# Kernel tuning notes

Measured on AMD Instinct MI355X. Metric: run time of the kernel, lower is better.

The kernel has to match this reference:

```python
import jax, jax.numpy as jnp
import numpy as np

B, H, W, C = 4, 64, 64, 256
C8 = C // 8

def setup_inputs() -> dict:
    key = jax.random.key(0)
    k1, k2, k3, k4 = jax.random.split(key, 4)
    # glorot-uniform-ish init for 1x1 conv kernels stored as [Cin, Cout]
    def glorot(k, cin, cout):
        lim = np.sqrt(6.0 / (cin + cout)).astype(np.float32)
        return jax.random.uniform(k, (cin, cout), jnp.float32, -lim, lim)
    return {
        "x": jax.random.normal(k1, (B, H, W, C), jnp.float32),
        "kernel_f": glorot(k2, C, C8),
        "kernel_g": glorot(k3, C, C8),
        "kernel_h": glorot(k4, C, C),
        "gamma": jnp.zeros((1,), jnp.float32),
    }

def reference(x, kernel_f, kernel_g, kernel_h, gamma):
    b, h, w, c = x.shape
    n = h * w
    xf = x.reshape(b, n, c)                       # [B, N, C]
    # 1x1 convs == per-position matmuls
    f = jnp.einsum('bnc,cd->bnd', xf, kernel_f)   # [B, N, C/8]
    g = jnp.einsum('bnc,cd->bnd', xf, kernel_g)   # [B, N, C/8]
    hh = jnp.einsum('bnc,cd->bnd', xf, kernel_h)  # [B, N, C]
    s = jnp.einsum('bnd,bmd->bnm', g, f)          # [B, N, N]
    beta = jax.nn.softmax(s, axis=-1)
    o = jnp.einsum('bnm,bmc->bnc', beta, hh)      # [B, N, C]
    o = o.reshape(b, h, w, c)
    return gamma * o + x
```

## Files before the change

### kernel.cpp

```cpp
#include <hip/hip_runtime.h>
#include <hip/hip_bf16.h>

typedef __bf16 bf16x8 __attribute__((ext_vector_type(8)));
typedef float f32x4 __attribute__((ext_vector_type(4)));
typedef float f32x16 __attribute__((ext_vector_type(16)));
typedef unsigned short u16;
typedef unsigned int u32;

__device__ __forceinline__ u16 f2bf_rne(float f){
  union { float f; u32 u; } v; v.f = f;
  u32 r = v.u + 0x7fffu + ((v.u >> 16) & 1u);
  return (u16)(r >> 16);
}
__device__ __forceinline__ u32 pack2(float a, float b){
  return __builtin_amdgcn_perm(__float_as_uint(a), __float_as_uint(b), 0x03020706u);
}
#define BARRIER_LGKM() asm volatile("s_waitcnt lgkmcnt(0)\n\ts_barrier" ::: "memory")

__global__ __launch_bounds__(512) void prep_kernel(
    const float* __restrict__ Wf, const float* __restrict__ Wg,
    const float* __restrict__ Wh, u16* __restrict__ Wfrag){
  const int cc = blockIdx.x;
  const int t = threadIdx.x;
  const int kk = t >> 6, lane = t & 63;
  const int L = lane & 15, quad = lane >> 4;
  const int n = cc * 16 + L;
  u32 pk[4];
  #pragma unroll
  for (int j2 = 0; j2 < 4; ++j2){
    float v[2];
    #pragma unroll
    for (int h = 0; h < 2; ++h){
      int k = kk * 32 + quad * 8 + j2 * 2 + h;
      if (n < 256)      v[h] = Wh[k * 256 + n];
      else if (n < 288) v[h] = Wf[k * 32 + (n - 256)];
      else              v[h] = Wg[k * 32 + (n - 288)];
    }
    pk[j2] = (u32)f2bf_rne(v[0]) | ((u32)f2bf_rne(v[1]) << 16);
  }
  uint4* dst = (uint4*)(Wfrag + ((size_t)(cc * 8 + kk) * 64 + lane) * 8);
  *dst = make_uint4(pk[0], pk[1], pk[2], pk[3]);
}

__global__ __launch_bounds__(512) void proj_kernel(
    const float* __restrict__ x, const u16* __restrict__ Wfrag,
    u16* __restrict__ Qg, u16* __restrict__ Kg, u16* __restrict__ Vfrag)
{
  __shared__ __align__(16) u16 smem[256 * 72];
  u16 (*xb)[264] = (u16(*)[264])smem;
  u16 (*Vr)[72]  = (u16(*)[72])smem;

  const int tid = threadIdx.x;
  const int lane = tid & 63, wave = tid >> 6;
  const int L = lane & 15, quad = lane >> 4;
  const int rowgrp = wave >> 1, colhalf = wave & 1;
  const int n0 = blockIdx.x * 64;

  const float4* xsrc = (const float4*)(x + (size_t)n0 * 256);
  #pragma unroll
  for (int j = 0; j < 8; ++j){
    int idx = j * 512 + tid;
    int row = idx >> 6, col4 = idx & 63;
    float4 v = xsrc[idx];
    u32 p0 = (u32)f2bf_rne(v.x) | ((u32)f2bf_rne(v.y) << 16);
    u32 p1 = (u32)f2bf_rne(v.z) | ((u32)f2bf_rne(v.w) << 16);
    *(uint2*)&xb[row][col4 * 4] = make_uint2(p0, p1);
  }
  __syncthreads();

  f32x4 acc[10];
  #pragma unroll
  for (int cc = 0; cc < 10; ++cc) acc[cc] = (f32x4){0.f, 0.f, 0.f, 0.f};

  #pragma unroll
  for (int kk = 0; kk < 8; ++kk){
    bf16x8 a = *(const bf16x8*)&xb[rowgrp * 16 + L][kk * 32 + quad * 8];
    #pragma unroll
    for (int cc = 0; cc < 10; ++cc){
      int ccg = colhalf * 10 + cc;
      bf16x8 bfr = *(const bf16x8*)(Wfrag + ((size_t)(ccg * 8 + kk) * 64 + lane) * 8);
      acc[cc] = __builtin_amdgcn_mfma_f32_16x16x32_bf16(a, bfr, acc[cc], 0, 0, 0);
    }
  }

  if (colhalf){
    #pragma unroll
    for (int cc = 6; cc < 10; ++cc){
      int ccg = 10 + cc;
      u16* dst = (ccg < 18) ? Kg : Qg;
      float sc = (ccg < 18) ? 1.0f : 1.44269504088896f;
      int c = (ccg & 1) * 16 + L;
      #pragma unroll
      for (int r = 0; r < 4; ++r){
        int row = n0 + rowgrp * 16 + quad * 4 + r;
        dst[(size_t)row * 32 + c] = f2bf_rne(acc[cc][r] * sc);
      }
    }
  }

  __syncthreads();

  {
    const int cmax = colhalf ? 6 : 10;
    for (int cc = 0; cc < cmax; ++cc){
      int ccg = colhalf * 10 + cc;
      int c = ccg * 16 + L;
      #pragma unroll
      for (int r = 0; r < 4; ++r){
        int tn = rowgrp * 16 + quad * 4 + r;
        int p  = ((tn & 15) << 2) | (tn >> 4);
        Vr[c][p] = f2bf_rne(acc[cc][r]);
      }
    }
  }
  __syncthreads();

  u16* Vblk = Vfrag + (size_t)blockIdx.x * (256 * 64);
  #pragma unroll
  for (int i = 0; i < 4; ++i){
    int idx = i * 512 + tid;
    *(uint4*)(Vblk + (size_t)idx * 8) = *(const uint4*)&Vr[idx & 255][(idx >> 8) * 8];
  }
}

__global__ __launch_bounds__(512) void flash_kernel(
    const u16* __restrict__ Qg, const u16* __restrict__ Kg, const u16* __restrict__ Vfrag,
    const float* __restrict__ x, const float* __restrict__ gamma, float* __restrict__ out)
{
  constexpr float SH = -92.33248261689366f;
  __shared__ __align__(16) char smem[65536];
  u16 (*Plds)[2][64][72] = (u16 (*)[2][64][72])smem;
  float (*Osh)[256] = (float (*)[256])smem;
  __shared__ float Lsh[64];

  const int tid = threadIdx.x, lane = tid & 63, wave = tid >> 6;
  const int L = lane & 15, quad = lane >> 4;
  const int m32 = lane & 31, h32 = lane >> 5;
  const bool producer = wave < 4;
  const int pw = wave & 3;

  const int id = blockIdx.x;
  const int xcd = id & 7;
  const int b = xcd >> 1;
  const int qt = (xcd & 1) * 32 + (id >> 3);
  const int q0 = qt * 64;

  const u16* Qb = Qg + (size_t)(b * 4096) * 32;
  const u16* Kb = Kg + (size_t)(b * 4096) * 32;
  const u16* Vb = Vfrag + (size_t)b * (64 * 256 * 64);
  const float gm = gamma[0];

  bf16x8 qa;
  bf16x8 kcA0, kcA1, kcA2, kcA3, kcB0, kcB1, kcB2, kcB3;
  bf16x8 vfA[8], vfB[8];
  if (producer){
    qa = *(const bf16x8*)(Qb + (size_t)(q0 + pw * 16 + L) * 32 + quad * 8);
    const u16* kpA = Kb + (size_t)(0 * 64 + L) * 32 + quad * 8;
    kcA0 = *(const bf16x8*)(kpA);
    kcA1 = *(const bf16x8*)(kpA + 512);
    kcA2 = *(const bf16x8*)(kpA + 1024);
    kcA3 = *(const bf16x8*)(kpA + 1536);
    const u16* kpB = kpA + 2048;
    kcB0 = *(const bf16x8*)(kpB);
    kcB1 = *(const bf16x8*)(kpB + 512);
    kcB2 = *(const bf16x8*)(kpB + 1024);
    kcB3 = *(const bf16x8*)(kpB + 1536);
  } else {
    #pragma unroll
    for (int ks = 0; ks < 4; ++ks){
      const u16* vrow = Vb + (size_t)((ks * 2 + h32) * 256 + pw * 64 + m32) * 8;
      vfA[ks * 2]     = *(const bf16x8*)(vrow);
      vfA[ks * 2 + 1] = *(const bf16x8*)(vrow + 32 * 8);
      vfB[ks * 2]     = *(const bf16x8*)(vrow + 16384);
      vfB[ks * 2 + 1] = *(const bf16x8*)(vrow + 16384 + 32 * 8);
    }
  }

  f32x16 acc[4];
  #pragma unroll
  for (int t = 0; t < 4; ++t)
    #pragma unroll
    for (int i = 0; i < 16; ++i) acc[t][i] = 0.f;
  float lsum[4] = {0.f, 0.f, 0.f, 0.f};
  const f32x4 zero = (f32x4){0.f, 0.f, 0.f, 0.f};

  for (int it = 0; it < 32; ++it){
    u16 (*PwA)[72] = Plds[it & 1][0];
    u16 (*PwB)[72] = Plds[it & 1][1];

    if (producer){
      f32x4 sA0 = __builtin_amdgcn_mfma_f32_16x16x32_bf16(qa, kcA0, zero, 0, 0, 0);
      f32x4 sA1 = __builtin_amdgcn_mfma_f32_16x16x32_bf16(qa, kcA1, zero, 0, 0, 0);
      f32x4 sA2 = __builtin_amdgcn_mfma_f32_16x16x32_bf16(qa, kcA2, zero, 0, 0, 0);
      f32x4 sA3 = __builtin_amdgcn_mfma_f32_16x16x32_bf16(qa, kcA3, zero, 0, 0, 0);
      f32x4 sB0 = __builtin_amdgcn_mfma_f32_16x16x32_bf16(qa, kcB0, zero, 0, 0, 0);
      f32x4 sB1 = __builtin_amdgcn_mfma_f32_16x16x32_bf16(qa, kcB1, zero, 0, 0, 0);
      f32x4 sB2 = __builtin_amdgcn_mfma_f32_16x16x32_bf16(qa, kcB2, zero, 0, 0, 0);
      f32x4 sB3 = __builtin_amdgcn_mfma_f32_16x16x32_bf16(qa, kcB3, zero, 0, 0, 0);

      if (it < 31){
        const u16* kpa = Kb + (size_t)((2 * it + 2) * 64 + L) * 32 + quad * 8;
        kcA0 = *(const bf16x8*)(kpa);
        kcA1 = *(const bf16x8*)(kpa + 512);
        kcA2 = *(const bf16x8*)(kpa + 1024);
        kcA3 = *(const bf16x8*)(kpa + 1536);
        const u16* kpb = kpa + 2048;
        kcB0 = *(const bf16x8*)(kpb);
        kcB1 = *(const bf16x8*)(kpb + 512);
        kcB2 = *(const bf16x8*)(kpb + 1024);
        kcB3 = *(const bf16x8*)(kpb + 1536);
      }

      #pragma unroll
      for (int r = 0; r < 4; ++r){
        float a0 = __builtin_amdgcn_exp2f(sA0[r] + SH);
        float a1 = __builtin_amdgcn_exp2f(sA1[r] + SH);
        float a2 = __builtin_amdgcn_exp2f(sA2[r] + SH);
        float a3 = __builtin_amdgcn_exp2f(sA3[r] + SH);
        float b0 = __builtin_amdgcn_exp2f(sB0[r] + SH);
        float b1 = __builtin_amdgcn_exp2f(sB1[r] + SH);
        float b2 = __builtin_amdgcn_exp2f(sB2[r] + SH);
        float b3 = __builtin_amdgcn_exp2f(sB3[r] + SH);
        lsum[r] += ((a0 + a1) + (a2 + a3)) + ((b0 + b1) + (b2 + b3));
        *(uint2*)&PwA[pw * 16 + quad * 4 + r][L * 4] =
            make_uint2(pack2(a0, a1), pack2(a2, a3));
        *(uint2*)&PwB[pw * 16 + quad * 4 + r][L * 4] =
            make_uint2(pack2(b0, b1), pack2(b2, b3));
      }
    }

    BARRIER_LGKM();

    if (!producer){
      #pragma unroll
      for (int ks = 0; ks < 4; ++ks){
        bf16x8 af0 = *(const bf16x8*)&PwA[m32][ks * 16 + h32 * 8];
        bf16x8 af1 = *(const bf16x8*)&PwA[32 + m32][ks * 16 + h32 * 8];
        acc[0] = __builtin_amdgcn_mfma_f32_32x32x16_bf16(af0, vfA[ks*2],   acc[0], 0, 0, 0);
        acc[1] = __builtin_amdgcn_mfma_f32_32x32x16_bf16(af0, vfA[ks*2+1], acc[1], 0, 0, 0);
        acc[2] = __builtin_amdgcn_mfma_f32_32x32x16_bf16(af1, vfA[ks*2],   acc[2], 0, 0, 0);
        acc[3] = __builtin_amdgcn_mfma_f32_32x32x16_bf16(af1, vfA[ks*2+1], acc[3], 0, 0, 0);
      }
      #pragma unroll
      for (int ks = 0; ks < 4; ++ks){
        bf16x8 af0 = *(const bf16x8*)&PwB[m32][ks * 16 + h32 * 8];
        bf16x8 af1 = *(const bf16x8*)&PwB[32 + m32][ks * 16 + h32 * 8];
        acc[0] = __builtin_amdgcn_mfma_f32_32x32x16_bf16(af0, vfB[ks*2],   acc[0], 0, 0, 0);
        acc[1] = __builtin_amdgcn_mfma_f32_32x32x16_bf16(af0, vfB[ks*2+1], acc[1], 0, 0, 0);
        acc[2] = __builtin_amdgcn_mfma_f32_32x32x16_bf16(af1, vfB[ks*2],   acc[2], 0, 0, 0);
        acc[3] = __builtin_amdgcn_mfma_f32_32x32x16_bf16(af1, vfB[ks*2+1], acc[3], 0, 0, 0);
      }
      if (it < 31){
        const u16* Vn = Vb + (size_t)(2 * it + 2) * (256 * 64);
        #pragma unroll
        for (int ks = 0; ks < 4; ++ks){
          const u16* vrow = Vn + (size_t)((ks * 2 + h32) * 256 + pw * 64 + m32) * 8;
          vfA[ks * 2]     = *(const bf16x8*)(vrow);
          vfA[ks * 2 + 1] = *(const bf16x8*)(vrow + 32 * 8);
          vfB[ks * 2]     = *(const bf16x8*)(vrow + 16384);
          vfB[ks * 2 + 1] = *(const bf16x8*)(vrow + 16384 + 32 * 8);
        }
      }
    }
  }

  BARRIER_LGKM();

  if (producer){
    #pragma unroll
    for (int r = 0; r < 4; ++r){
      lsum[r] += __shfl_xor(lsum[r], 1);
      lsum[r] += __shfl_xor(lsum[r], 2);
      lsum[r] += __shfl_xor(lsum[r], 4);
      lsum[r] += __shfl_xor(lsum[r], 8);
    }
    if (L == 0){
      #pragma unroll
      for (int r = 0; r < 4; ++r) Lsh[pw * 16 + quad * 4 + r] = lsum[r];
    }
  } else {
    #pragma unroll
    for (int t = 0; t < 4; ++t){
      const int qi = t >> 1, ci = t & 1;
      #pragma unroll
      for (int rg = 0; rg < 16; ++rg){
        int row = qi * 32 + (rg & 3) + 8 * (rg >> 2) + 4 * h32;
        Osh[row][pw * 64 + ci * 32 + m32] = acc[t][rg];
      }
    }
  }
  __syncthreads();
  if (wave == 0) Lsh[lane] = gm / Lsh[lane];
  __syncthreads();
  const size_t base = ((size_t)(b * 4096) + q0) * 256;
  const float4* xs = (const float4*)(x + base);
  float4* od = (float4*)(out + base);
  const float4* Of = (const float4*)&Osh[0][0];
  #pragma unroll
  for (int i = 0; i < 8; ++i){
    int idx = i * 512 + tid;
    float li = Lsh[idx >> 6];
    float4 o = Of[idx], xv = xs[idx];
    o.x = o.x * li + xv.x; o.y = o.y * li + xv.y;
    o.z = o.z * li + xv.z; o.w = o.w * li + xv.w;
    od[idx] = o;
  }
}

extern "C" void kernel_launch(void* const* d_in, const int* in_sizes, int n_in,
                              void* d_out, int out_size, void* d_ws, size_t ws_size,
                              hipStream_t stream) {
  const float* x     = (const float*)d_in[0];
  const float* Wf    = (const float*)d_in[1];
  const float* Wg    = (const float*)d_in[2];
  const float* Wh    = (const float*)d_in[3];
  const float* gamma = (const float*)d_in[4];
  float* out = (float*)d_out;

  u16* p = (u16*)d_ws;
  u16* Qg    = p;  p += 16384 * 32;
  u16* Kg    = p;  p += 16384 * 32;
  u16* Vfrag = p;  p += 4 * 64 * 256 * 64;
  u16* Wfrag = p;  p += 20 * 8 * 64 * 8;

  prep_kernel<<<20, 512, 0, stream>>>(Wf, Wg, Wh, Wfrag);
  proj_kernel<<<256, 512, 0, stream>>>(x, Wfrag, Qg, Kg, Vfrag);
  flash_kernel<<<256, 512, 0, stream>>>(Qg, Kg, Vfrag, x, gamma, out);
}
```

Baseline: 148.7 us.

## Retile flash kernel to 128 query rows by 128 output channels per block

Each block now covers 128 query rows and half of the 256 output channels instead of 64 rows and all channels, so two blocks share each query tile and split the channel dimension. Each consumer wave keeps half as many V fragments in registers, and each P fragment read from LDS is reused across one accumulator instead of two. Producers compute twice as many score tiles and exps per block, and the exp/QK work is duplicated across the two channel-half blocks. LDS use grows to 72KB, which may limit occupancy.

```diff
diff --git a/kernel.cpp b/kernel.cpp
--- a/kernel.cpp
+++ b/kernel.cpp
@@ -128,10 +128,10 @@
     const float* __restrict__ x, const float* __restrict__ gamma, float* __restrict__ out)
 {
   constexpr float SH = -92.33248261689366f;
-  __shared__ __align__(16) char smem[65536];
-  u16 (*Plds)[2][64][72] = (u16 (*)[2][64][72])smem;
-  float (*Osh)[256] = (float (*)[256])smem;
-  __shared__ float Lsh[64];
+  __shared__ __align__(16) char smem[73728];
+  u16 (*Plds)[2][128][72] = (u16 (*)[2][128][72])smem;
+  float (*Osh)[128] = (float (*)[128])smem;
+  __shared__ float Lsh[128];
 
   const int tid = threadIdx.x, lane = tid & 63, wave = tid >> 6;
   const int L = lane & 15, quad = lane >> 4;
@@ -142,19 +142,23 @@
   const int id = blockIdx.x;
   const int xcd = id & 7;
   const int b = xcd >> 1;
-  const int qt = (xcd & 1) * 32 + (id >> 3);
-  const int q0 = qt * 64;
+  const int ch = (id >> 3) & 1;
+  const int qt = (xcd & 1) * 16 + (id >> 4);
+  const int q0 = qt * 128;
 
   const u16* Qb = Qg + (size_t)(b * 4096) * 32;
   const u16* Kb = Kg + (size_t)(b * 4096) * 32;
   const u16* Vb = Vfrag + (size_t)b * (64 * 256 * 64);
   const float gm = gamma[0];
 
-  bf16x8 qa;
+  const int ccol = ch * 128 + pw * 32 + m32;
+
+  bf16x8 qa0, qa1;
   bf16x8 kcA0, kcA1, kcA2, kcA3, kcB0, kcB1, kcB2, kcB3;
-  bf16x8 vfA[8], vfB[8];
+  bf16x8 vfA[4], vfB[4];
   if (producer){
-    qa = *(const bf16x8*)(Qb + (size_t)(q0 + pw * 16 + L) * 32 + quad * 8);
+    qa0 = *(const bf16x8*)(Qb + (size_t)(q0 + pw * 32 + L) * 32 + quad * 8);
+    qa1 = *(const bf16x8*)(Qb + (size_t)(q0 + pw * 32 + 16 + L) * 32 + quad * 8);
     const u16* kpA = Kb + (size_t)(0 * 64 + L) * 32 + quad * 8;
     kcA0 = *(const bf16x8*)(kpA);
     kcA1 = *(const bf16x8*)(kpA + 512);
@@ -168,11 +172,9 @@
   } else {
     #pragma unroll
     for (int ks = 0; ks < 4; ++ks){
-      const u16* vrow = Vb + (size_t)((ks * 2 + h32) * 256 + pw * 64 + m32) * 8;
-      vfA[ks * 2]     = *(const bf16x8*)(vrow);
-      vfA[ks * 2 + 1] = *(const bf16x8*)(vrow + 32 * 8);
-      vfB[ks * 2]     = *(const bf16x8*)(vrow + 16384);
-      vfB[ks * 2 + 1] = *(const bf16x8*)(vrow + 16384 + 32 * 8);
+      const u16* vrow = Vb + (size_t)((ks * 2 + h32) * 256 + ccol) * 8;
+      vfA[ks] = *(const bf16x8*)(vrow);
+      vfB[ks] = *(const bf16x8*)(vrow + 16384);
     }
   }
 
@@ -181,7 +183,7 @@
   for (int t = 0; t < 4; ++t)
     #pragma unroll
     for (int i = 0; i < 16; ++i) acc[t][i] = 0.f;
-  float lsum[4] = {0.f, 0.f, 0.f, 0.f};
+  float lsum[2][4] = {{0.f,0.f,0.f,0.f},{0.f,0.f,0.f,0.f}};
   const f32x4 zero = (f32x4){0.f, 0.f, 0.f, 0.f};
 
   for (int it = 0; it < 32; ++it){
@@ -189,14 +191,19 @@
     u16 (*PwB)[72] = Plds[it & 1][1];
 
     if (producer){
-      f32x4 sA0 = __builtin_amdgcn_mfma_f32_16x16x32_bf16(qa, kcA0, zero, 0, 0, 0);
-      f32x4 sA1 = __builtin_amdgcn_mfma_f32_16x16x32_bf16(qa, kcA1, zero, 0, 0, 0);
-      f32x4 sA2 = __builtin_amdgcn_mfma_f32_16x16x32_bf16(qa, kcA2, zero, 0, 0, 0);
-      f32x4 sA3 = __builtin_amdgcn_mfma_f32_16x16x32_bf16(qa, kcA3, zero, 0, 0, 0);
-      f32x4 sB0 = __builtin_amdgcn_mfma_f32_16x16x32_bf16(qa, kcB0, zero, 0, 0, 0);
-      f32x4 sB1 = __builtin_amdgcn_mfma_f32_16x16x32_bf16(qa, kcB1, zero, 0, 0, 0);
-      f32x4 sB2 = __builtin_amdgcn_mfma_f32_16x16x32_bf16(qa, kcB2, zero, 0, 0, 0);
-      f32x4 sB3 = __builtin_amdgcn_mfma_f32_16x16x32_bf16(qa, kcB3, zero, 0, 0, 0);
+      f32x4 sA[2][4], sB[2][4];
+      #pragma unroll
+      for (int qg = 0; qg < 2; ++qg){
+        bf16x8 q = qg ? qa1 : qa0;
+        sA[qg][0] = __builtin_amdgcn_mfma_f32_16x16x32_bf16(q, kcA0, zero, 0, 0, 0);
+        sA[qg][1] = __builtin_amdgcn_mfma_f32_16x16x32_bf16(q, kcA1, zero, 0, 0, 0);
+        sA[qg][2] = __builtin_amdgcn_mfma_f32_16x16x32_bf16(q, kcA2, zero, 0, 0, 0);
+        sA[qg][3] = __builtin_amdgcn_mfma_f32_16x16x32_bf16(q, kcA3, zero, 0, 0, 0);
+        sB[qg][0] = __builtin_amdgcn_mfma_f32_16x16x32_bf16(q, kcB0, zero, 0, 0, 0);
+        sB[qg][1] = __builtin_amdgcn_mfma_f32_16x16x32_bf16(q, kcB1, zero, 0, 0, 0);
+        sB[qg][2] = __builtin_amdgcn_mfma_f32_16x16x32_bf16(q, kcB2, zero, 0, 0, 0);
+        sB[qg][3] = __builtin_amdgcn_mfma_f32_16x16x32_bf16(q, kcB3, zero, 0, 0, 0);
+      }
 
       if (it < 31){
         const u16* kpa = Kb + (size_t)((2 * it + 2) * 64 + L) * 32 + quad * 8;
@@ -212,20 +219,22 @@
       }
 
       #pragma unroll
-      for (int r = 0; r < 4; ++r){
-        float a0 = __builtin_amdgcn_exp2f(sA0[r] + SH);
-        float a1 = __builtin_amdgcn_exp2f(sA1[r] + SH);
-        float a2 = __builtin_amdgcn_exp2f(sA2[r] + SH);
-        float a3 = __builtin_amdgcn_exp2f(sA3[r] + SH);
-        float b0 = __builtin_amdgcn_exp2f(sB0[r] + SH);
-        float b1 = __builtin_amdgcn_exp2f(sB1[r] + SH);
-        float b2 = __builtin_amdgcn_exp2f(sB2[r] + SH);
-        float b3 = __builtin_amdgcn_exp2f(sB3[r] + SH);
-        lsum[r] += ((a0 + a1) + (a2 + a3)) + ((b0 + b1) + (b2 + b3));
-        *(uint2*)&PwA[pw * 16 + quad * 4 + r][L * 4] =
-            make_uint2(pack2(a0, a1), pack2(a2, a3));
-        *(uint2*)&PwB[pw * 16 + quad * 4 + r][L * 4] =
-            make_uint2(pack2(b0, b1), pack2(b2, b3));
+      for (int qg = 0; qg < 2; ++qg){
+        #pragma unroll
+        for (int r = 0; r < 4; ++r){
+          float a0 = __builtin_amdgcn_exp2f(sA[qg][0][r] + SH);
+          float a1 = __builtin_amdgcn_exp2f(sA[qg][1][r] + SH);
+          float a2 = __builtin_amdgcn_exp2f(sA[qg][2][r] + SH);
+          float a3 = __builtin_amdgcn_exp2f(sA[qg][3][r] + SH);
+          float b0 = __builtin_amdgcn_exp2f(sB[qg][0][r] + SH);
+          float b1 = __builtin_amdgcn_exp2f(sB[qg][1][r] + SH);
+          float b2 = __builtin_amdgcn_exp2f(sB[qg][2][r] + SH);
+          float b3 = __builtin_amdgcn_exp2f(sB[qg][3][r] + SH);
+          lsum[qg][r] += ((a0 + a1) + (a2 + a3)) + ((b0 + b1) + (b2 + b3));
+          int row = pw * 32 + qg * 16 + quad * 4 + r;
+          *(uint2*)&PwA[row][L * 4] = make_uint2(pack2(a0, a1), pack2(a2, a3));
+          *(uint2*)&PwB[row][L * 4] = make_uint2(pack2(b0, b1), pack2(b2, b3));
+        }
       }
     }
 
@@ -233,32 +242,25 @@
 
     if (!producer){
       #pragma unroll
-      for (int ks = 0; ks < 4; ++ks){
-        bf16x8 af0 = *(const bf16x8*)&PwA[m32][ks * 16 + h32 * 8];
-        bf16x8 af1 = *(const bf16x8*)&PwA[32 + m32][ks * 16 + h32 * 8];
-        acc[0] = __builtin_amdgcn_mfma_f32_32x32x16_bf16(af0, vfA[ks*2],   acc[0], 0, 0, 0);
-        acc[1] = __builtin_amdgcn_mfma_f32_32x32x16_bf16(af0, vfA[ks*2+1], acc[1], 0, 0, 0);
-        acc[2] = __builtin_amdgcn_mfma_f32_32x32x16_bf16(af1, vfA[ks*2],   acc[2], 0, 0, 0);
-        acc[3] = __builtin_amdgcn_mfma_f32_32x32x16_bf16(af1, vfA[ks*2+1], acc[3], 0, 0, 0);
-      }
-      #pragma unroll
-      for (int ks = 0; ks < 4; ++ks){
-        bf16x8 af0 = *(const bf16x8*)&PwB[m32][ks * 16 + h32 * 8];
-        bf16x8 af1 = *(const bf16x8*)&PwB[32 + m32][ks * 16 + h32 * 8];
-        acc[0] = __builtin_amdgcn_mfma_f32_32x32x16_bf16(af0, vfB[ks*2],   acc[0], 0, 0, 0);
-        acc[1] = __builtin_amdgcn_mfma_f32_32x32x16_bf16(af0, vfB[ks*2+1], acc[1], 0, 0, 0);
-        acc[2] = __builtin_amdgcn_mfma_f32_32x32x16_bf16(af1, vfB[ks*2],   acc[2], 0, 0, 0);
-        acc[3] = __builtin_amdgcn_mfma_f32_32x32x16_bf16(af1, vfB[ks*2+1], acc[3], 0, 0, 0);
+      for (int qi = 0; qi < 4; ++qi){
+        #pragma unroll
+        for (int ks = 0; ks < 4; ++ks){
+          bf16x8 af = *(const bf16x8*)&PwA[qi * 32 + m32][ks * 16 + h32 * 8];
+          acc[qi] = __builtin_amdgcn_mfma_f32_32x32x16_bf16(af, vfA[ks], acc[qi], 0, 0, 0);
+        }
+        #pragma unroll
+        for (int ks = 0; ks < 4; ++ks){
+          bf16x8 af = *(const bf16x8*)&PwB[qi * 32 + m32][ks * 16 + h32 * 8];
+          acc[qi] = __builtin_amdgcn_mfma_f32_32x32x16_bf16(af, vfB[ks], acc[qi], 0, 0, 0);
+        }
       }
       if (it < 31){
         const u16* Vn = Vb + (size_t)(2 * it + 2) * (256 * 64);
         #pragma unroll
         for (int ks = 0; ks < 4; ++ks){
-          const u16* vrow = Vn + (size_t)((ks * 2 + h32) * 256 + pw * 64 + m32) * 8;
-          vfA[ks * 2]     = *(const bf16x8*)(vrow);
-          vfA[ks * 2 + 1] = *(const bf16x8*)(vrow + 32 * 8);
-          vfB[ks * 2]     = *(const bf16x8*)(vrow + 16384);
-          vfB[ks * 2 + 1] = *(const bf16x8*)(vrow + 16384 + 32 * 8);
+          const u16* vrow = Vn + (size_t)((ks * 2 + h32) * 256 + ccol) * 8;
+          vfA[ks] = *(const bf16x8*)(vrow);
+          vfB[ks] = *(const bf16x8*)(vrow + 16384);
         }
       }
     }
@@ -268,42 +270,42 @@
 
   if (producer){
     #pragma unroll
-    for (int r = 0; r < 4; ++r){
-      lsum[r] += __shfl_xor(lsum[r], 1);
-      lsum[r] += __shfl_xor(lsum[r], 2);
-      lsum[r] += __shfl_xor(lsum[r], 4);
-      lsum[r] += __shfl_xor(lsum[r], 8);
-    }
-    if (L == 0){
-      #pragma unroll
-      for (int r = 0; r < 4; ++r) Lsh[pw * 16 + quad * 4 + r] = lsum[r];
+    for (int qg = 0; qg < 2; ++qg){
+      #pragma unroll
+      for (int r = 0; r < 4; ++r){
+        float v = lsum[qg][r];
+        v += __shfl_xor(v, 1);
+        v += __shfl_xor(v, 2);
+        v += __shfl_xor(v, 4);
+        v += __shfl_xor(v, 8);
+        if (L == 0) Lsh[pw * 32 + qg * 16 + quad * 4 + r] = v;
+      }
     }
   } else {
     #pragma unroll
-    for (int t = 0; t < 4; ++t){
-      const int qi = t >> 1, ci = t & 1;
+    for (int qi = 0; qi < 4; ++qi){
       #pragma unroll
       for (int rg = 0; rg < 16; ++rg){
-        int row = qi * 32 + (rg & 3) + 8 * (rg >> 2) + 4 * h32;
-        Osh[row][pw * 64 + ci * 32 + m32] = acc[t][rg];
-      }
-    }
-  }
-  __syncthreads();
-  if (wave == 0) Lsh[lane] = gm / Lsh[lane];
-  __syncthreads();
-  const size_t base = ((size_t)(b * 4096) + q0) * 256;
-  const float4* xs = (const float4*)(x + base);
-  float4* od = (float4*)(out + base);
-  const float4* Of = (const float4*)&Osh[0][0];
+        int crow = (rg & 3) + 8 * (rg >> 2) + 4 * h32;
+        Osh[qi * 32 + crow][pw * 32 + m32] = acc[qi][rg];
+      }
+    }
+  }
+  __syncthreads();
+  if (tid < 128) Lsh[tid] = gm / Lsh[tid];
+  __syncthreads();
+  const size_t base = ((size_t)(b * 4096 + q0)) * 256 + ch * 128;
   #pragma unroll
   for (int i = 0; i < 8; ++i){
     int idx = i * 512 + tid;
-    float li = Lsh[idx >> 6];
-    float4 o = Of[idx], xv = xs[idx];
+    int row = idx >> 5, c4 = idx & 31;
+    size_t off = base + (size_t)row * 256 + c4 * 4;
+    float li = Lsh[row];
+    float4 o = *(const float4*)&Osh[row][c4 * 4];
+    float4 xv = *(const float4*)(x + off);
     o.x = o.x * li + xv.x; o.y = o.y * li + xv.y;
     o.z = o.z * li + xv.z; o.w = o.w * li + xv.w;
-    od[idx] = o;
+    *(float4*)(out + off) = o;
   }
 }
 
```

Result: slower. 151.9 us (+2.2%).
